# Kernel optimization log

Hardware: AMD Instinct MI355X
Metric: run time of the kernel (lower is better)

Reference implementation:

```python
import jax, jax.numpy as jnp
import numpy as np


def _pairwise_upper_dists(x):
    # x: [N, D] -> distances for all i<j pairs, shape [N*(N-1)/2]
    n = x.shape[0]
    sq = jnp.sum(x * x, axis=-1)                      # [N]
    d2 = sq[:, None] + sq[None, :] - 2.0 * (x @ x.T)  # [N, N]
    d2 = jnp.maximum(d2, 0.0)
    iu, ju = jnp.triu_indices(n, k=1)                 # matches combinations(range(n), 2)
    return jnp.sqrt(d2[iu, ju])


def setup_inputs() -> dict:
    key = jax.random.key(0)
    k1, k2 = jax.random.split(key)
    pred = jax.random.normal(k1, (1024, 8192), dtype=jnp.float32)
    target = jax.random.normal(k2, (1024, 8192), dtype=jnp.float32)
    return {"pred": pred, "target": target}


def reference(pred, target):
    # all_pairs_in_batch=True branch: Euclidean distance per pair, MSE between
    # the pred-distance vector and the target-distance vector.
    pred_d = _pairwise_upper_dists(pred)      # [P]
    target_d = _pairwise_upper_dists(target)  # [P]
    return jnp.mean((pred_d - target_d) ** 2)
```

## Files before the change

### kernel.cpp

```cpp
#include <hip/hip_runtime.h>
#include <hip/hip_bf16.h>
#include <hip/hip_fp16.h>

#define D 8192
#define NPAIR 523776.0

typedef short short8 __attribute__((ext_vector_type(8)));
typedef float f32x4 __attribute__((ext_vector_type(4)));
typedef _Float16 f16x8 __attribute__((ext_vector_type(8)));
typedef int int32x4 __attribute__((ext_vector_type(4)));

#define GLOAD_LDS(G, L) __builtin_amdgcn_global_load_lds( \
    (const __attribute__((address_space(1))) void*)(G),   \
    (__attribute__((address_space(3))) void*)(L), 16, 0, 0)

__device__ __forceinline__ short8 cvt8(const float4 a, const float4 b) {
    union { short8 s; __hip_bfloat162 h[4]; } u;
    u.h[0] = __float22bfloat162_rn(make_float2(a.x, a.y));
    u.h[1] = __float22bfloat162_rn(make_float2(a.z, a.w));
    u.h[2] = __float22bfloat162_rn(make_float2(b.x, b.y));
    u.h[3] = __float22bfloat162_rn(make_float2(b.z, b.w));
    return u.s;
}

__device__ __forceinline__ int q8(float x) {
    return __float2int_rn(fminf(fmaxf(x * 32.f, -127.f), 127.f));
}
__device__ __forceinline__ int pack4(float a, float b, float c, float d) {
    return (q8(a) & 255) | ((q8(b) & 255) << 8) | ((q8(c) & 255) << 16) | ((q8(d) & 255) << 24);
}

__device__ __forceinline__ void decode_bid(int bid, int& m, int& ti, int& tj, int& k0, int& nsteps) {
    int x = bid & 7, s = bid >> 3;
    m = x >> 2;
    int xr = x & 3;
    if (s < 16) {
        ti = tj = s & 7;
        int c = ((s >> 3) << 2) + xr;
        k0 = c * 1024; nsteps = 16;
    } else {
        int sp = s - 16;
        int c = (sp / 28) * 4 + xr;
        int tt = sp % 28;
        int a = 0;
        while (tt >= 7 - a) { tt -= 7 - a; ++a; }
        ti = a; tj = a + 1 + tt;
        k0 = c * 512; nsteps = 8;
    }
}
__device__ __forceinline__ int bid_off(int m, int tt, int c) {
    return (m * 4 + (c & 3)) + ((16 + (c >> 2) * 28 + tt) << 3);
}
__device__ __forceinline__ int bid_diag(int m, int dt, int c) {
    return (m * 4 + (c & 3)) + ((((c >> 2) << 3) + dt) << 3);
}

__global__ __launch_bounds__(256)
void convert_kernel(const float* __restrict__ pred, const float* __restrict__ tgt,
                    char* __restrict__ q) {
    const int idx = blockIdx.x * 256 + threadIdx.x;
    const int t = idx & 511;
    const int c = idx >> 9;
    const int m = c >> 10, p = (c >> 7) & 7, ks = c & 127;
    const int rl = t >> 2;
    const int s = (t & 3) ^ ((rl >> 1) & 3);
    const float* __restrict__ src = (m ? tgt : pred) + (size_t)(p * 128 + rl) * D + ks * 64 + s * 16;
    const float4 a = ((const float4*)src)[0];
    const float4 b = ((const float4*)src)[1];
    const float4 e = ((const float4*)src)[2];
    const float4 f = ((const float4*)src)[3];
    int32x4 o;
    o[0] = pack4(a.x, a.y, a.z, a.w);
    o[1] = pack4(b.x, b.y, b.z, b.w);
    o[2] = pack4(e.x, e.y, e.z, e.w);
    o[3] = pack4(f.x, f.y, f.z, f.w);
    *(int32x4*)(q + (size_t)c * 8192 + t * 16) = o;
}

#define STAGE(S, COFF) { \
    GLOAD_LDS(gAc + (size_t)(S) * 8192 + gsub, lsb + (COFF) + wid * 1024); \
    if (!same) GLOAD_LDS(gBc + (size_t)(S) * 8192 + gsub, lsb + (COFF) + 8192 + wid * 1024); \
}

#define GSTEP { \
    if (sp + 1 < nsteps) STAGE(sp + 1, cN); \
    { \
        const char* __restrict__ bA = lsb + cC; \
        const char* __restrict__ bB = lsb + cC + boff; \
        __builtin_amdgcn_s_setprio(1); \
        int32x4 b0 = *(const int32x4*)(bB + rbB + kby); \
        int32x4 b1 = *(const int32x4*)(bB + rbB + 1024 + kby); \
        _Pragma("unroll") \
        for (int mi = 0; mi < 4; ++mi) { \
            int32x4 af = *(const int32x4*)(bA + rbA + mi * 1024 + kby); \
            acc[mi][0] = __builtin_amdgcn_mfma_i32_16x16x64_i8(af, b0, acc[mi][0], 0, 0, 0); \
            acc[mi][1] = __builtin_amdgcn_mfma_i32_16x16x64_i8(af, b1, acc[mi][1], 0, 0, 0); \
        } \
        __builtin_amdgcn_s_setprio(0); \
    } \
    asm volatile("s_waitcnt vmcnt(0)" ::: "memory"); \
    __builtin_amdgcn_s_barrier(); \
    { int t_ = cC; cC = cN; cN = t_; } \
    ++sp; \
}

__global__ __launch_bounds__(512, 8)
void gram_kernel(const char* __restrict__ q, __half* __restrict__ part,
                 float* __restrict__ norms) {
    int m, ti, tj, k0, nsteps;
    decode_bid(blockIdx.x, m, ti, tj, k0, nsteps);
    const bool same = (ti == tj);

    __shared__ short ls[16384];
    char* lsb = (char*)ls;

    const int tid = threadIdx.x;
    const int lane = tid & 63;
    const int wid = tid >> 6;
    const int wr = wid >> 2, wc = wid & 3;

    const char* __restrict__ gAc = q + (size_t)(m * 1024 + ti * 128 + (k0 >> 6)) * 8192;
    const char* __restrict__ gBc = q + (size_t)(m * 1024 + tj * 128 + (k0 >> 6)) * 8192;
    const int gsub = wid * 1024 + lane * 16;

    const int boff = same ? 0 : 8192;
    const int rbA = (wr * 64 + (lane & 15)) * 64;
    const int rbB = (wc * 32 + (lane & 15)) * 64;
    const int kby = (((lane >> 4) ^ (((lane & 15) >> 1) & 3)) << 4);

    int32x4 zero = {0, 0, 0, 0};
    int32x4 acc[4][2];
#pragma unroll
    for (int mi = 0; mi < 4; ++mi) { acc[mi][0] = zero; acc[mi][1] = zero; }

    int cC = 0, cN = 16384;

    STAGE(0, cC)
    asm volatile("s_waitcnt vmcnt(0)" ::: "memory");
    __builtin_amdgcn_s_barrier();

    int sp = 0;
    while (sp < nsteps) { GSTEP }

    if (same) {
#pragma unroll
        for (int mi = 0; mi < 4; ++mi)
#pragma unroll
            for (int ni = 0; ni < 2; ++ni)
#pragma unroll
                for (int r = 0; r < 4; ++r) {
                    int li = wr * 64 + mi * 16 + (lane >> 4) * 4 + r;
                    int lj = wc * 32 + ni * 16 + (lane & 15);
                    if (li == lj)
                        atomicAdd(&norms[m * 1024 + ti * 128 + li],
                                  (float)acc[mi][ni][r] * (1.f / 1024.f));
                }
    }
    __syncthreads();
#pragma unroll
    for (int mi = 0; mi < 4; ++mi)
#pragma unroll
        for (int ni = 0; ni < 2; ++ni)
#pragma unroll
            for (int r = 0; r < 4; ++r) {
                int li = wr * 64 + mi * 16 + (lane >> 4) * 4 + r;
                int lj = wc * 32 + ni * 16 + (lane & 15);
                int byte = li * 256 + ((lj * 2) ^ ((li & 7) << 4));
                *(__half*)(lsb + byte) = __float2half_rn((float)acc[mi][ni][r] * (1.f / 1024.f));
            }
    __syncthreads();
    char* __restrict__ dstb = (char*)(part + (size_t)blockIdx.x * 16384);
#pragma unroll
    for (int qq = 0; qq < 4; ++qq) {
        int L = qq * 8192 + tid * 16;
        int li = L >> 8;
        f16x8 v = *(const f16x8*)(lsb + (L ^ ((li & 7) << 4)));
        *(f16x8*)(dstb + L) = v;
    }
}

__global__ __launch_bounds__(256)
void loss_store_kernel(const __half* __restrict__ part, const float* __restrict__ norms,
                       float* __restrict__ partial) {
    const int tid = threadIdx.x;
    const int sid = blockIdx.x * 256 + tid;
    const int i  = sid >> 7;
    const int j0 = (sid & 127) << 3;
    float local = 0.f;
    if (j0 + 7 > i) {
        const int ti = i >> 7, tj = j0 >> 7;
        const int el = ((i & 127) << 7) + (j0 & 127);
        float gp[8] = {0,0,0,0,0,0,0,0}, gt[8] = {0,0,0,0,0,0,0,0};
        if (ti == tj) {
#pragma unroll
            for (int c = 0; c < 8; ++c) {
                f16x8 vp = *(const f16x8*)(part + (size_t)bid_diag(0, ti, c) * 16384 + el);
                f16x8 vt = *(const f16x8*)(part + (size_t)bid_diag(1, ti, c) * 16384 + el);
#pragma unroll
                for (int e = 0; e < 8; ++e) { gp[e] += (float)vp[e]; gt[e] += (float)vt[e]; }
            }
        } else {
            int tt = 7 * ti - (ti * (ti - 1)) / 2 + (tj - ti - 1);
#pragma unroll
            for (int c = 0; c < 16; ++c) {
                f16x8 vp = *(const f16x8*)(part + (size_t)bid_off(0, tt, c) * 16384 + el);
                f16x8 vt = *(const f16x8*)(part + (size_t)bid_off(1, tt, c) * 16384 + el);
#pragma unroll
                for (int e = 0; e < 8; ++e) { gp[e] += (float)vp[e]; gt[e] += (float)vt[e]; }
            }
        }
        const float nip = norms[i], nit = norms[1024 + i];
        const float4 njp0 = *(const float4*)(norms + j0);
        const float4 njp1 = *(const float4*)(norms + j0 + 4);
        const float4 njt0 = *(const float4*)(norms + 1024 + j0);
        const float4 njt1 = *(const float4*)(norms + 1024 + j0 + 4);
        const float njp[8] = {njp0.x, njp0.y, njp0.z, njp0.w, njp1.x, njp1.y, njp1.z, njp1.w};
        const float njt[8] = {njt0.x, njt0.y, njt0.z, njt0.w, njt1.x, njt1.y, njt1.z, njt1.w};
#pragma unroll
        for (int e = 0; e < 8; ++e) {
            int j = j0 + e;
            if (j > i) {
                float dp = nip + njp[e] - 2.f * gp[e];
                float dt = nit + njt[e] - 2.f * gt[e];
                float c2 = sqrtf(fmaxf(dp, 0.f)) - sqrtf(fmaxf(dt, 0.f));
                local += c2 * c2;
            }
        }
    }
#pragma unroll
    for (int off = 32; off > 0; off >>= 1) local += __shfl_down(local, off);
    __shared__ float wsum[4];
    if ((tid & 63) == 0) wsum[tid >> 6] = local;
    __syncthreads();
    if (tid == 0) partial[blockIdx.x] = wsum[0] + wsum[1] + wsum[2] + wsum[3];
}

template<int NPART>
__global__ __launch_bounds__(256)
void finalize_kernel(const float* __restrict__ partial, float* __restrict__ out) {
    const int tid = threadIdx.x;
    double local = 0.0;
#pragma unroll
    for (int k = 0; k < NPART / 256; ++k) local += (double)partial[tid + k * 256];
#pragma unroll
    for (int off = 32; off > 0; off >>= 1) local += __shfl_down(local, off);
    __shared__ double wsum[4];
    if ((tid & 63) == 0) wsum[tid >> 6] = local;
    __syncthreads();
    if (tid == 0) out[0] = (float)((wsum[0] + wsum[1] + wsum[2] + wsum[3]) / NPAIR);
}

__device__ __forceinline__ void decode_bid_fb(int bid, int& m, int& ti, int& tj, int& k0, int& nsteps) {
    int x = bid & 7, s = bid >> 3;
    m = x >> 2;
    int xr = x & 3;
    if (s < 16) {
        ti = tj = s & 7;
        int c = ((s >> 3) << 2) + xr;
        k0 = c * 1024; nsteps = 32;
    } else {
        int sp = s - 16;
        int c = (sp / 28) * 4 + xr;
        int tt = sp % 28;
        int a = 0;
        while (tt >= 7 - a) { tt -= 7 - a; ++a; }
        ti = a; tj = a + 1 + tt;
        k0 = c * 512; nsteps = 16;
    }
}

__global__ __launch_bounds__(512)
void gram_fb(const float* __restrict__ pred, const float* __restrict__ tgt,
             float* __restrict__ g4) {
    int m, ti, tj, k0, nsteps;
    decode_bid_fb(blockIdx.x, m, ti, tj, k0, nsteps);
    const bool same = (ti == tj);
    const float* __restrict__ x = m ? tgt : pred;
    __shared__ short lsA[2][4096];
    __shared__ short lsB[2][4096];
    const int tid = threadIdx.x;
    const int lane = tid & 63;
    const int wid = tid >> 6;
    const int wr = wid >> 2, wc = wid & 3;
    const int srow = tid >> 2, sc8 = tid & 3;
    const float* __restrict__ gA = x + (size_t)(ti * 128 + srow) * D + k0 + sc8 * 8;
    const float* __restrict__ gB = x + (size_t)(tj * 128 + srow) * D + k0 + sc8 * 8;
    const int wby = srow * 64 + ((sc8 ^ ((srow >> 1) & 3)) << 4);
    const int rbA = (wr * 64 + (lane & 15)) * 64;
    const int rbB = (wc * 32 + (lane & 15)) * 64;
    const int kby = (((lane >> 4) ^ (((lane & 15) >> 1) & 3)) << 4);
    f32x4 zero = {0.f, 0.f, 0.f, 0.f};
    f32x4 acc[4][2];
#pragma unroll
    for (int mi = 0; mi < 4; ++mi) { acc[mi][0] = zero; acc[mi][1] = zero; }
    float4 ra0, ra1, rb0, rb1;
    { const float4* p = (const float4*)gA; ra0 = p[0]; ra1 = p[1];
      if (!same) { const float4* qq = (const float4*)gB; rb0 = qq[0]; rb1 = qq[1]; } }
    *(short8*)((char*)lsA[0] + wby) = cvt8(ra0, ra1);
    if (!same) *(short8*)((char*)lsB[0] + wby) = cvt8(rb0, rb1);
    { const float4* p = (const float4*)(gA + 32); ra0 = p[0]; ra1 = p[1];
      if (!same) { const float4* qq = (const float4*)(gB + 32); rb0 = qq[0]; rb1 = qq[1]; } }
    asm volatile("s_waitcnt lgkmcnt(0)" ::: "memory");
    __builtin_amdgcn_s_barrier();
    for (int step = 0; step < nsteps; ++step) {
        const int cur = step & 1;
        const short* __restrict__ bufA = lsA[cur];
        const short* __restrict__ bufB = same ? lsA[cur] : lsB[cur];
        short8 bf0 = *(const short8*)((const char*)bufB + (rbB + kby));
        short8 bf1 = *(const short8*)((const char*)bufB + (rbB + 1024 + kby));
#pragma unroll
        for (int mi = 0; mi < 4; ++mi) {
            short8 af = *(const short8*)((const char*)bufA + (rbA + mi * 1024 + kby));
            acc[mi][0] = __builtin_amdgcn_mfma_f32_16x16x32_bf16(af, bf0, acc[mi][0], 0, 0, 0);
            acc[mi][1] = __builtin_amdgcn_mfma_f32_16x16x32_bf16(af, bf1, acc[mi][1], 0, 0, 0);
        }
        if (step + 1 < nsteps) {
            const int nxt = cur ^ 1;
            *(short8*)((char*)lsA[nxt] + wby) = cvt8(ra0, ra1);
            if (!same) *(short8*)((char*)lsB[nxt] + wby) = cvt8(rb0, rb1);
            if (step + 2 < nsteps) {
                const float4* p = (const float4*)(gA + (step + 2) * 32);
                ra0 = p[0]; ra1 = p[1];
                if (!same) { const float4* qq = (const float4*)(gB + (step + 2) * 32); rb0 = qq[0]; rb1 = qq[1]; }
            }
        }
        asm volatile("s_waitcnt lgkmcnt(0)" ::: "memory");
        __builtin_amdgcn_s_barrier();
    }
#pragma unroll
    for (int mi = 0; mi < 4; ++mi)
#pragma unroll
        for (int ni = 0; ni < 2; ++ni)
#pragma unroll
            for (int r = 0; r < 4; ++r) {
                int gi = ti * 128 + wr * 64 + mi * 16 + (lane >> 4) * 4 + r;
                int gj = tj * 128 + wc * 32 + ni * 16 + (lane & 15);
                atomicAdd(&g4[(size_t)m * 1048576 + gi * 1024 + gj], acc[mi][ni][r]);
            }
}

__global__ __launch_bounds__(256)
void loss_atomic_kernel(const float* __restrict__ gram, float* __restrict__ partial) {
    const float* __restrict__ gP = gram;
    const float* __restrict__ gT = gram + 1024 * 1024;
    const int tid = threadIdx.x;
    const int base = blockIdx.x * 256 + tid;
    float local = 0.f;
#pragma unroll
    for (int s = 0; s < 4; ++s) {
        int lin = base + s * 262144;
        int i = lin >> 10, j = lin & 1023;
        if (j > i) {
            float dp = gP[i * 1024 + i] + gP[j * 1024 + j] - 2.f * gP[lin];
            float dt = gT[i * 1024 + i] + gT[j * 1024 + j] - 2.f * gT[lin];
            float c = sqrtf(fmaxf(dp, 0.f)) - sqrtf(fmaxf(dt, 0.f));
            local += c * c;
        }
    }
#pragma unroll
    for (int off = 32; off > 0; off >>= 1) local += __shfl_down(local, off);
    __shared__ float wsum[4];
    if ((tid & 63) == 0) wsum[tid >> 6] = local;
    __syncthreads();
    if (tid == 0) partial[blockIdx.x] = wsum[0] + wsum[1] + wsum[2] + wsum[3];
}

extern "C" void kernel_launch(void* const* d_in, const int* in_sizes, int n_in,
                              void* d_out, int out_size, void* d_ws, size_t ws_size,
                              hipStream_t stream) {
    const float* pred = (const float*)d_in[0];
    const float* tgt  = (const float*)d_in[1];
    const size_t q_bytes    = (size_t)2048 * 8192;
    const size_t part_bytes = (size_t)1024 * 16384 * 2;
    const size_t need = q_bytes + part_bytes + (2048 + 512) * sizeof(float);
    if (ws_size >= need) {
        char* qbuf     = (char*)d_ws;
        __half* part   = (__half*)((char*)d_ws + q_bytes);
        float* norms   = (float*)((char*)part + part_bytes);
        float* partial = norms + 2048;
        hipMemsetAsync(norms, 0, 2048 * sizeof(float), stream);
        convert_kernel<<<4096, 256, 0, stream>>>(pred, tgt, qbuf);
        gram_kernel<<<1024, 512, 0, stream>>>(qbuf, part, norms);
        loss_store_kernel<<<512, 256, 0, stream>>>(part, norms, partial);
        finalize_kernel<512><<<1, 256, 0, stream>>>(partial, (float*)d_out);
    } else {
        float* gram    = (float*)d_ws;
        float* partial = (float*)d_ws + (size_t)2 * 1024 * 1024;
        hipMemsetAsync(gram, 0, (size_t)2 * 1024 * 1024 * sizeof(float), stream);
        gram_fb<<<1024, 512, 0, stream>>>(pred, tgt, gram);
        loss_atomic_kernel<<<1024, 256, 0, stream>>>(gram, partial);
        finalize_kernel<1024><<<1, 256, 0, stream>>>(partial, (float*)d_out);
    }
}
```

Baseline: 47.88 us.

## Load int8 MFMA operands directly from global into double-buffered registers

Removes the LDS staging path (global_load_lds plus a barrier each k-step) from the int8 Gram kernel. Each wave now loads its own A and B fragments straight from global memory into two register sets and alternates MFMA work on one set with loads into the other. Launch bounds drop to 4 blocks per CU to leave room for the extra registers. This trades the barrier and LDS round-trip for redundant global/L2 reads, since waves that share a tile row or column fetch the same data. The unrolled loop also assumes nsteps is even and at least two.

```diff
diff --git a/kernel.cpp b/kernel.cpp
--- a/kernel.cpp
+++ b/kernel.cpp
@@ -9,10 +9,6 @@
 typedef float f32x4 __attribute__((ext_vector_type(4)));
 typedef _Float16 f16x8 __attribute__((ext_vector_type(8)));
 typedef int int32x4 __attribute__((ext_vector_type(4)));
-
-#define GLOAD_LDS(G, L) __builtin_amdgcn_global_load_lds( \
-    (const __attribute__((address_space(1))) void*)(G),   \
-    (__attribute__((address_space(3))) void*)(L), 16, 0, 0)
 
 __device__ __forceinline__ short8 cvt8(const float4 a, const float4 b) {
     union { short8 s; __hip_bfloat162 h[4]; } u;
@@ -77,34 +73,26 @@
     *(int32x4*)(q + (size_t)c * 8192 + t * 16) = o;
 }
 
-#define STAGE(S, COFF) { \
-    GLOAD_LDS(gAc + (size_t)(S) * 8192 + gsub, lsb + (COFF) + wid * 1024); \
-    if (!same) GLOAD_LDS(gBc + (size_t)(S) * 8192 + gsub, lsb + (COFF) + 8192 + wid * 1024); \
-}
-
-#define GSTEP { \
-    if (sp + 1 < nsteps) STAGE(sp + 1, cN); \
-    { \
-        const char* __restrict__ bA = lsb + cC; \
-        const char* __restrict__ bB = lsb + cC + boff; \
-        __builtin_amdgcn_s_setprio(1); \
-        int32x4 b0 = *(const int32x4*)(bB + rbB + kby); \
-        int32x4 b1 = *(const int32x4*)(bB + rbB + 1024 + kby); \
-        _Pragma("unroll") \
-        for (int mi = 0; mi < 4; ++mi) { \
-            int32x4 af = *(const int32x4*)(bA + rbA + mi * 1024 + kby); \
-            acc[mi][0] = __builtin_amdgcn_mfma_i32_16x16x64_i8(af, b0, acc[mi][0], 0, 0, 0); \
-            acc[mi][1] = __builtin_amdgcn_mfma_i32_16x16x64_i8(af, b1, acc[mi][1], 0, 0, 0); \
-        } \
-        __builtin_amdgcn_s_setprio(0); \
+#define LOADSTEP(S, RA, RB) { \
+    const char* pa_ = gAc + (size_t)(S) * 8192; \
+    RA[0] = *(const int32x4*)(pa_ + rbA + kby); \
+    RA[1] = *(const int32x4*)(pa_ + rbA + 1024 + kby); \
+    RA[2] = *(const int32x4*)(pa_ + rbA + 2048 + kby); \
+    RA[3] = *(const int32x4*)(pa_ + rbA + 3072 + kby); \
+    const char* pb_ = gBc + (size_t)(S) * 8192; \
+    RB[0] = *(const int32x4*)(pb_ + rbB + kby); \
+    RB[1] = *(const int32x4*)(pb_ + rbB + 1024 + kby); \
+}
+
+#define MFMASTEP(RA, RB) { \
+    _Pragma("unroll") \
+    for (int mi = 0; mi < 4; ++mi) { \
+        acc[mi][0] = __builtin_amdgcn_mfma_i32_16x16x64_i8(RA[mi], RB[0], acc[mi][0], 0, 0, 0); \
+        acc[mi][1] = __builtin_amdgcn_mfma_i32_16x16x64_i8(RA[mi], RB[1], acc[mi][1], 0, 0, 0); \
     } \
-    asm volatile("s_waitcnt vmcnt(0)" ::: "memory"); \
-    __builtin_amdgcn_s_barrier(); \
-    { int t_ = cC; cC = cN; cN = t_; } \
-    ++sp; \
-}
-
-__global__ __launch_bounds__(512, 8)
+}
+
+__global__ __launch_bounds__(512, 4)
 void gram_kernel(const char* __restrict__ q, __half* __restrict__ part,
                  float* __restrict__ norms) {
     int m, ti, tj, k0, nsteps;
@@ -121,9 +109,7 @@
 
     const char* __restrict__ gAc = q + (size_t)(m * 1024 + ti * 128 + (k0 >> 6)) * 8192;
     const char* __restrict__ gBc = q + (size_t)(m * 1024 + tj * 128 + (k0 >> 6)) * 8192;
-    const int gsub = wid * 1024 + lane * 16;
-
-    const int boff = same ? 0 : 8192;
+
     const int rbA = (wr * 64 + (lane & 15)) * 64;
     const int rbB = (wc * 32 + (lane & 15)) * 64;
     const int kby = (((lane >> 4) ^ (((lane & 15) >> 1) & 3)) << 4);
@@ -133,14 +119,17 @@
 #pragma unroll
     for (int mi = 0; mi < 4; ++mi) { acc[mi][0] = zero; acc[mi][1] = zero; }
 
-    int cC = 0, cN = 16384;
-
-    STAGE(0, cC)
-    asm volatile("s_waitcnt vmcnt(0)" ::: "memory");
-    __builtin_amdgcn_s_barrier();
-
-    int sp = 0;
-    while (sp < nsteps) { GSTEP }
+    int32x4 aX[4], bX[2], aY[4], bY[2];
+    LOADSTEP(0, aX, bX)
+    LOADSTEP(1, aY, bY)
+    for (int sp = 0; sp + 2 < nsteps; sp += 2) {
+        MFMASTEP(aX, bX)
+        LOADSTEP(sp + 2, aX, bX)
+        MFMASTEP(aY, bY)
+        if (sp + 3 < nsteps) LOADSTEP(sp + 3, aY, bY)
+    }
+    MFMASTEP(aX, bX)
+    MFMASTEP(aY, bY)
 
     if (same) {
 #pragma unroll
@@ -156,7 +145,6 @@
                                   (float)acc[mi][ni][r] * (1.f / 1024.f));
                 }
     }
-    __syncthreads();
 #pragma unroll
     for (int mi = 0; mi < 4; ++mi)
 #pragma unroll
```

Measured after the change: 54.38 us. 1.14x slower.
